# Performance work log

Measured on AMD Instinct MI355X. Metric: run time of the kernel, lower is better.

The kernel has to match this reference:

```python
import jax, jax.numpy as jnp
import numpy as np

DIM = 1024
HEADS = 16
HEAD_DIM = DIM // HEADS
SCALE = DIM ** -0.5  # note: original uses full dim, not head_dim


def setup_inputs() -> dict:
    key = jax.random.key(0)
    k1, k2, k3, k4 = jax.random.split(key, 4)
    x = jax.random.normal(k1, (4, 2048, DIM), dtype=jnp.float32)
    # nn.Linear(dim, 3*dim, bias=False): weight [3*dim, dim]; y = x @ W.T
    w_qkv = jax.random.normal(k2, (3 * DIM, DIM), dtype=jnp.float32) * (DIM ** -0.5)
    w_out = jax.random.normal(k3, (DIM, DIM), dtype=jnp.float32) * (DIM ** -0.5)
    b_out = jax.random.normal(k4, (DIM,), dtype=jnp.float32) * 0.01
    return {"x": x, "w_qkv": w_qkv, "w_out": w_out, "b_out": b_out}


def reference(x, w_qkv, w_out, b_out):
    b, n, d = x.shape
    qkv = jnp.einsum('bnd,ed->bne', x, w_qkv)  # [b, n, 3*dim]
    # rearrange 'b n (qkv h d) -> qkv b h n d'
    qkv = qkv.reshape(b, n, 3, HEADS, HEAD_DIM).transpose(2, 0, 3, 1, 4)
    q, k, v = qkv[0], qkv[1], qkv[2]
    dots = jnp.einsum('bhid,bhjd->bhij', q, k) * SCALE
    attn = jax.nn.softmax(dots, axis=-1)
    out = jnp.einsum('bhij,bhjd->bhid', attn, v)
    out = out.transpose(0, 2, 1, 3).reshape(b, n, d)  # b h n d -> b n (h d)
    return jnp.einsum('bnd,ed->bne', out, w_out) + b_out
```

## Files before the change

kernel.cpp:

```cpp
#include <hip/hip_runtime.h>
#include <stdint.h>
#include <stddef.h>

typedef _Float16 f16;
typedef __attribute__((ext_vector_type(8))) _Float16 f16x8;
typedef __attribute__((ext_vector_type(4))) _Float16 f16x4;
typedef __attribute__((ext_vector_type(4))) float f32x4;

#define DINL __device__ __forceinline__

DINL void async_cp16(void* lds, const void* gmem) {
    __builtin_amdgcn_global_load_lds(
        (const __attribute__((address_space(1))) void*)(uintptr_t)gmem,
        (__attribute__((address_space(3))) void*)(uint32_t)(uintptr_t)lds,
        16, 0, 0);
}

__global__ void cast_fused(const float* __restrict__ x, f16* __restrict__ xh,
                           const float* __restrict__ wq, f16* __restrict__ wqh,
                           const float* __restrict__ wo, f16* __restrict__ woh,
                           float qs) {
    int stride = gridDim.x * blockDim.x;
    for (int i = blockIdx.x * blockDim.x + threadIdx.x; i < 3145728; i += stride) {
        const float4* src; f16x4* dst; float s = 1.f;
        if (i < 2097152)      { src = (const float4*)x  + i;            dst = (f16x4*)xh  + i; }
        else if (i < 2883584) { int j = i - 2097152; src = (const float4*)wq + j; dst = (f16x4*)wqh + j;
                                if (j < 262144) s = qs; }
        else                  { int j = i - 2883584; src = (const float4*)wo + j; dst = (f16x4*)woh + j; }
        float4 v = *src;
        f16x4 h = { (f16)(v.x * s), (f16)(v.y * s), (f16)(v.z * s), (f16)(v.w * s) };
        *dst = h;
    }
}

template <typename TC, bool HAS_BIAS>
__global__ __launch_bounds__(256) void gemm_bt(
    const f16* __restrict__ A, const f16* __restrict__ B,
    TC* __restrict__ C, const float* __restrict__ bias,
    int M, int N, int K)
{
    constexpr int BK = 64;
    __shared__ __align__(16) f16 As[128 * BK];
    __shared__ __align__(16) f16 Bs[128 * BK];

    const int tid  = threadIdx.x;
    const int lane = tid & 63;
    const int wave = tid >> 6;
    const int bm = blockIdx.y * 128;
    const int bn = blockIdx.x * 128;
    const int wr = (wave >> 1) * 64;
    const int wc = (wave & 1) * 64;

    f32x4 acc[4][4] = {};

    for (int k0 = 0; k0 < K; k0 += BK) {
#pragma unroll
        for (int it = 0; it < 4; ++it) {
            int s = tid + it * 256, row = s >> 3, cc = (s & 7) ^ (row & 7);
            async_cp16(&As[(size_t)s * 8], &A[(size_t)(bm + row) * K + k0 + cc * 8]);
        }
#pragma unroll
        for (int it = 0; it < 4; ++it) {
            int s = tid + it * 256, row = s >> 3, cc = (s & 7) ^ (row & 7);
            async_cp16(&Bs[(size_t)s * 8], &B[(size_t)(bn + row) * K + k0 + cc * 8]);
        }
        __syncthreads();

#pragma unroll
        for (int ks = 0; ks < BK; ks += 32) {
            const int rlo = lane & 15;
            const int c = (ks >> 3) + (lane >> 4);
            f16x8 af[4], bf[4];
#pragma unroll
            for (int m = 0; m < 4; ++m) {
                int r = wr + m * 16 + rlo;
                af[m] = *(const f16x8*)&As[(r * 8 + (c ^ (r & 7))) * 8];
            }
#pragma unroll
            for (int n = 0; n < 4; ++n) {
                int r = wc + n * 16 + rlo;
                bf[n] = *(const f16x8*)&Bs[(r * 8 + (c ^ (r & 7))) * 8];
            }
#pragma unroll
            for (int m = 0; m < 4; ++m)
#pragma unroll
                for (int n = 0; n < 4; ++n)
                    acc[m][n] = __builtin_amdgcn_mfma_f32_16x16x32_f16(af[m], bf[n], acc[m][n], 0, 0, 0);
        }
        __syncthreads();
    }

#pragma unroll
    for (int n = 0; n < 4; ++n) {
        const int gc = bn + wc + n * 16 + (lane & 15);
        float bv = 0.f;
        if constexpr (HAS_BIAS) bv = bias[gc];
#pragma unroll
        for (int m = 0; m < 4; ++m) {
            const int gr0 = bm + wr + m * 16 + ((lane >> 4) << 2);
#pragma unroll
            for (int r = 0; r < 4; ++r) {
                float v = acc[m][n][r] + bv;
                if constexpr (sizeof(TC) == 4) C[(size_t)(gr0 + r) * N + gc] = v;
                else                           C[(size_t)(gr0 + r) * N + gc] = (f16)v;
            }
        }
    }
}

__global__ __launch_bounds__(256) void transpose_v(const f16* __restrict__ qkv, f16* __restrict__ vt) {
    __shared__ float T[64][65];
    const int bid = blockIdx.x, bh = bid >> 5, st = bid & 31;
    const int b = bh >> 4, h = bh & 15, s0 = st * 64;
    const int tid = threadIdx.x;
    const int rs = tid >> 2, c0 = (tid & 3) * 16;
    const f16* src = &qkv[(size_t)(b * 2048 + s0 + rs) * 3072 + 2048 + h * 64 + c0];
    f16x8 v0 = ((const f16x8*)src)[0], v1 = ((const f16x8*)src)[1];
#pragma unroll
    for (int e = 0; e < 8; ++e) { T[rs][c0 + e] = (float)v0[e]; T[rs][c0 + 8 + e] = (float)v1[e]; }
    __syncthreads();
    const int rd = tid >> 2, k0 = (tid & 3) * 16;
    f16x8 w0, w1;
#pragma unroll
    for (int e = 0; e < 8; ++e) { w0[e] = (f16)T[k0 + e][rd]; w1[e] = (f16)T[k0 + 8 + e][rd]; }
    f16* dst = &vt[(size_t)(bh * 64 + rd) * 2048 + s0 + k0];
    ((f16x8*)dst)[0] = w0; ((f16x8*)dst)[1] = w1;
}

DINL int phi_row(int r) {
    return (r & 32) | ((r & 12) << 1) | ((r & 16) >> 2) | (r & 3);
}

__global__ __launch_bounds__(256, 5) void attn_mfma(
    const f16* __restrict__ qkv, const f16* __restrict__ vt, f16* __restrict__ out)
{
    constexpr int TD = 3072;
    constexpr int KSTR = 64 * TD;
    __shared__ __align__(16) f16 Ks[2][64 * 64];
    __shared__ __align__(16) f16 Vs[2][64 * 64];

    const int tid = threadIdx.x, lane = tid & 63, wave = tid >> 6;
    const int bh = blockIdx.x, b = bh >> 4, h = bh & 15;
    const int q0 = blockIdx.y * 64;
    const size_t base = (size_t)b * 2048 * TD + h * 64;
    const int lo = lane & 15, hi = lane >> 4;

    const f16* qp = &qkv[base + (size_t)(q0 + wave * 16 + lo) * TD + hi * 8];
    f16x8 qf0 = *(const f16x8*)qp;
    f16x8 qf1 = *(const f16x8*)(qp + 32);

    const int s1 = tid,        r1 = s1 >> 3, c1 = (s1 & 7) ^ (r1 & 7);
    const int s2 = tid + 256,  r2 = s2 >> 3, c2 = (s2 & 7) ^ (r2 & 7);
    const f16* kg1 = &qkv[base + 1024 + (size_t)phi_row(r1) * TD + c1 * 8];
    const f16* kg2 = &qkv[base + 1024 + (size_t)phi_row(r2) * TD + c2 * 8];
    const f16* vg1 = &vt[(size_t)(bh * 64 + r1) * 2048 + c1 * 8];
    const f16* vg2 = &vt[(size_t)(bh * 64 + r2) * 2048 + c2 * 8];
    f16* kd1 = &Ks[0][s1 * 8]; f16* kd2 = &Ks[0][s2 * 8];
    f16* vd1 = &Vs[0][s1 * 8]; f16* vd2 = &Vs[0][s2 * 8];

    async_cp16(kd1, kg1); async_cp16(kd2, kg2);
    async_cp16(vd1, vg1); async_cp16(vd2, vg2);
    kg1 += KSTR; kg2 += KSTR; vg1 += 64; vg2 += 64;

    float lsum = 0.f;
    f32x4 o_[4] = {};

    for (int jt = 0; jt < 32; ++jt) {
        const int cur = jt & 1;
        __syncthreads();
        if (jt + 1 < 32) {
            const int nb = (cur ^ 1) * 4096;
            async_cp16(kd1 + nb, kg1); async_cp16(kd2 + nb, kg2);
            async_cp16(vd1 + nb, vg1); async_cp16(vd2 + nb, vg2);
            kg1 += KSTR; kg2 += KSTR; vg1 += 64; vg2 += 64;
        }

        f32x4 sc[4] = {};
#pragma unroll
        for (int ks = 0; ks < 2; ++ks) {
            const int c = ks * 4 + hi;
            const f16x8 qf = ks ? qf1 : qf0;
#pragma unroll
            for (int n = 0; n < 4; ++n) {
                int kr = n * 16 + lo;
                f16x8 kf = *(const f16x8*)&Ks[cur][(kr * 8 + (c ^ (kr & 7))) * 8];
                sc[n] = __builtin_amdgcn_mfma_f32_16x16x32_f16(kf, qf, sc[n], 0, 0, 0);
            }
        }

        f16x8 pa0, pa1;
#pragma unroll
        for (int n = 0; n < 4; ++n) {
            float p0 = exp2f(sc[n][0]), p1 = exp2f(sc[n][1]);
            float p2 = exp2f(sc[n][2]), p3 = exp2f(sc[n][3]);
            lsum += (p0 + p1) + (p2 + p3);
            const int off = (n & 1) * 4;
            if (n < 2) { pa0[off] = (f16)p0; pa0[off+1] = (f16)p1; pa0[off+2] = (f16)p2; pa0[off+3] = (f16)p3; }
            else       { pa1[off] = (f16)p0; pa1[off+1] = (f16)p1; pa1[off+2] = (f16)p2; pa1[off+3] = (f16)p3; }
        }

#pragma unroll
        for (int ks = 0; ks < 2; ++ks) {
            const int c = ks * 4 + hi;
            const f16x8 pa = ks ? pa1 : pa0;
#pragma unroll
            for (int n = 0; n < 4; ++n) {
                int dd = n * 16 + lo;
                f16x8 vb = *(const f16x8*)&Vs[cur][(dd * 8 + (c ^ (dd & 7))) * 8];
                o_[n] = __builtin_amdgcn_mfma_f32_16x16x32_f16(pa, vb, o_[n], 0, 0, 0);
            }
        }
    }

    lsum += __shfl_xor(lsum, 16);
    lsum += __shfl_xor(lsum, 32);
#pragma unroll
    for (int r = 0; r < 4; ++r) {
        float inv = 1.f / __shfl(lsum, hi * 4 + r);
        int row = q0 + wave * 16 + hi * 4 + r;
#pragma unroll
        for (int n = 0; n < 4; ++n) {
            int dim = h * 64 + n * 16 + lo;
            out[(size_t)(b * 2048 + row) * 1024 + dim] = (f16)(o_[n][r] * inv);
        }
    }
}

extern "C" void kernel_launch(void* const* d_in, const int* in_sizes, int n_in,
                              void* d_out, int out_size, void* d_ws, size_t ws_size,
                              hipStream_t stream)
{
    int ix = 0, iq = 1, iw = 2, ib = 3;
    for (int i = 0; i < n_in; ++i) {
        if      (in_sizes[i] == 8388608) ix = i;
        else if (in_sizes[i] == 3145728) iq = i;
        else if (in_sizes[i] == 1048576) iw = i;
        else if (in_sizes[i] == 1024)    ib = i;
    }
    const float* x     = (const float*)d_in[ix];
    const float* w_qkv = (const float*)d_in[iq];
    const float* w_out = (const float*)d_in[iw];
    const float* b_out = (const float*)d_in[ib];

    char* ws = (char*)d_ws;
    f16* Xh    = (f16*)(ws + 0);
    f16* AOh   = Xh;
    f16* Wqkvh = (f16*)(ws + 16777216);
    f16* QKVh  = (f16*)(ws + 23068672);
    f16* Vth   = (f16*)(ws + 73400320);
    f16* Wouth = (f16*)(ws + 90177536);

    const float QSCALE = 0.03125f * 1.4426950408889634f;

    cast_fused<<<3072, 256, 0, stream>>>(x, Xh, w_qkv, Wqkvh, w_out, Wouth, QSCALE);

    gemm_bt<f16, false><<<dim3(24, 64), 256, 0, stream>>>(
        Xh, Wqkvh, QKVh, nullptr, 8192, 3072, 1024);

    transpose_v<<<2048, 256, 0, stream>>>(QKVh, Vth);

    attn_mfma<<<dim3(64, 32), 256, 0, stream>>>(QKVh, Vth, AOh);

    gemm_bt<float, true><<<dim3(8, 64), 256, 0, stream>>>(
        AOh, Wouth, (float*)d_out, b_out, 8192, 1024, 1024);
}
```

Before: 290.3 us.

## Process two 16-row query groups per wave in attention kernel

```diff
diff --git a/kernel.cpp b/kernel.cpp
--- a/kernel.cpp
+++ b/kernel.cpp
@@ -131,7 +131,7 @@
     return (r & 32) | ((r & 12) << 1) | ((r & 16) >> 2) | (r & 3);
 }
 
-__global__ __launch_bounds__(256, 5) void attn_mfma(
+__global__ __launch_bounds__(256, 4) void attn_mfma(
     const f16* __restrict__ qkv, const f16* __restrict__ vt, f16* __restrict__ out)
 {
     constexpr int TD = 3072;
@@ -141,13 +141,17 @@
 
     const int tid = threadIdx.x, lane = tid & 63, wave = tid >> 6;
     const int bh = blockIdx.x, b = bh >> 4, h = bh & 15;
-    const int q0 = blockIdx.y * 64;
+    const int q0 = blockIdx.y * 128;
     const size_t base = (size_t)b * 2048 * TD + h * 64;
     const int lo = lane & 15, hi = lane >> 4;
 
-    const f16* qp = &qkv[base + (size_t)(q0 + wave * 16 + lo) * TD + hi * 8];
-    f16x8 qf0 = *(const f16x8*)qp;
-    f16x8 qf1 = *(const f16x8*)(qp + 32);
+    f16x8 qf[2][2];
+#pragma unroll
+    for (int g = 0; g < 2; ++g) {
+        const f16* qp = &qkv[base + (size_t)(q0 + wave * 32 + g * 16 + lo) * TD + hi * 8];
+        qf[g][0] = *(const f16x8*)qp;
+        qf[g][1] = *(const f16x8*)(qp + 32);
+    }
 
     const int s1 = tid,        r1 = s1 >> 3, c1 = (s1 & 7) ^ (r1 & 7);
     const int s2 = tid + 256,  r2 = s2 >> 3, c2 = (s2 & 7) ^ (r2 & 7);
@@ -162,8 +166,8 @@
     async_cp16(vd1, vg1); async_cp16(vd2, vg2);
     kg1 += KSTR; kg2 += KSTR; vg1 += 64; vg2 += 64;
 
-    float lsum = 0.f;
-    f32x4 o_[4] = {};
+    float lsum[2] = {};
+    f32x4 o_[2][4] = {};
 
     for (int jt = 0; jt < 32; ++jt) {
         const int cur = jt & 1;
@@ -175,53 +179,60 @@
             kg1 += KSTR; kg2 += KSTR; vg1 += 64; vg2 += 64;
         }
 
-        f32x4 sc[4] = {};
+        f32x4 sc[2][4] = {{}, {}};
 #pragma unroll
         for (int ks = 0; ks < 2; ++ks) {
             const int c = ks * 4 + hi;
-            const f16x8 qf = ks ? qf1 : qf0;
 #pragma unroll
             for (int n = 0; n < 4; ++n) {
                 int kr = n * 16 + lo;
                 f16x8 kf = *(const f16x8*)&Ks[cur][(kr * 8 + (c ^ (kr & 7))) * 8];
-                sc[n] = __builtin_amdgcn_mfma_f32_16x16x32_f16(kf, qf, sc[n], 0, 0, 0);
-            }
-        }
-
-        f16x8 pa0, pa1;
+                sc[0][n] = __builtin_amdgcn_mfma_f32_16x16x32_f16(kf, qf[0][ks], sc[0][n], 0, 0, 0);
+                sc[1][n] = __builtin_amdgcn_mfma_f32_16x16x32_f16(kf, qf[1][ks], sc[1][n], 0, 0, 0);
+            }
+        }
+
+        f16x8 pa[2][2];
+#pragma unroll
+        for (int g = 0; g < 2; ++g)
 #pragma unroll
         for (int n = 0; n < 4; ++n) {
-            float p0 = exp2f(sc[n][0]), p1 = exp2f(sc[n][1]);
-            float p2 = exp2f(sc[n][2]), p3 = exp2f(sc[n][3]);
-            lsum += (p0 + p1) + (p2 + p3);
+            float p0 = exp2f(sc[g][n][0]), p1 = exp2f(sc[g][n][1]);
+            float p2 = exp2f(sc[g][n][2]), p3 = exp2f(sc[g][n][3]);
+            lsum[g] += (p0 + p1) + (p2 + p3);
             const int off = (n & 1) * 4;
-            if (n < 2) { pa0[off] = (f16)p0; pa0[off+1] = (f16)p1; pa0[off+2] = (f16)p2; pa0[off+3] = (f16)p3; }
-            else       { pa1[off] = (f16)p0; pa1[off+1] = (f16)p1; pa1[off+2] = (f16)p2; pa1[off+3] = (f16)p3; }
+            const int w = n >> 1;
+            pa[g][w][off]   = (f16)p0; pa[g][w][off+1] = (f16)p1;
+            pa[g][w][off+2] = (f16)p2; pa[g][w][off+3] = (f16)p3;
         }
 
 #pragma unroll
         for (int ks = 0; ks < 2; ++ks) {
             const int c = ks * 4 + hi;
-            const f16x8 pa = ks ? pa1 : pa0;
 #pragma unroll
             for (int n = 0; n < 4; ++n) {
                 int dd = n * 16 + lo;
                 f16x8 vb = *(const f16x8*)&Vs[cur][(dd * 8 + (c ^ (dd & 7))) * 8];
-                o_[n] = __builtin_amdgcn_mfma_f32_16x16x32_f16(pa, vb, o_[n], 0, 0, 0);
-            }
-        }
-    }
-
-    lsum += __shfl_xor(lsum, 16);
-    lsum += __shfl_xor(lsum, 32);
-#pragma unroll
-    for (int r = 0; r < 4; ++r) {
-        float inv = 1.f / __shfl(lsum, hi * 4 + r);
-        int row = q0 + wave * 16 + hi * 4 + r;
-#pragma unroll
-        for (int n = 0; n < 4; ++n) {
-            int dim = h * 64 + n * 16 + lo;
-            out[(size_t)(b * 2048 + row) * 1024 + dim] = (f16)(o_[n][r] * inv);
+                o_[0][n] = __builtin_amdgcn_mfma_f32_16x16x32_f16(pa[0][ks], vb, o_[0][n], 0, 0, 0);
+                o_[1][n] = __builtin_amdgcn_mfma_f32_16x16x32_f16(pa[1][ks], vb, o_[1][n], 0, 0, 0);
+            }
+        }
+    }
+
+#pragma unroll
+    for (int g = 0; g < 2; ++g) {
+        float ls = lsum[g];
+        ls += __shfl_xor(ls, 16);
+        ls += __shfl_xor(ls, 32);
+#pragma unroll
+        for (int r = 0; r < 4; ++r) {
+            float inv = 1.f / __shfl(ls, hi * 4 + r);
+            int row = q0 + wave * 32 + g * 16 + hi * 4 + r;
+#pragma unroll
+            for (int n = 0; n < 4; ++n) {
+                int dim = h * 64 + n * 16 + lo;
+                out[(size_t)(b * 2048 + row) * 1024 + dim] = (f16)(o_[g][n][r] * inv);
+            }
         }
     }
 }
@@ -259,7 +270,7 @@
 
     transpose_v<<<2048, 256, 0, stream>>>(QKVh, Vth);
 
-    attn_mfma<<<dim3(64, 32), 256, 0, stream>>>(QKVh, Vth, AOh);
+    attn_mfma<<<dim3(64, 16), 256, 0, stream>>>(QKVh, Vth, AOh);
 
     gemm_bt<float, true><<<dim3(8, 64), 256, 0, stream>>>(
         AOh, Wouth, (float*)d_out, b_out, 8192, 1024, 1024);
```

New measurement: 297.2 us. 1.02x slower.
